# Kernel optimization log

Measured on AMD Instinct MI355X. Metric: run time of the kernel, lower is better.

## Reference

```python
import jax, jax.numpy as jnp
import numpy as np

Z = 16384      # batch of points
N_IN = 127     # dim(Rs_in)
N = N_IN + 1   # +1 ones channel since linear=True
K = 128        # dim(Rs_out)
DIM_TS = 2080  # dim(Rs_ts), ~ n(n+1)/2 surviving tensor-square paths
T_DENSITY = 0.05  # CG-like tensor T is sparse


def setup_inputs() -> dict:
    key = jax.random.key(0)
    k1, k2, k3, k4 = jax.random.split(key, 4)
    features = jax.random.normal(k1, (Z, N_IN), dtype=jnp.float32)
    W = jax.random.normal(k2, (K, DIM_TS), dtype=jnp.float32)  # KernelLinear weights
    T = jax.random.normal(k3, (DIM_TS, N * N), dtype=jnp.float32)
    mask = jax.random.uniform(k4, (DIM_TS, N * N)) < T_DENSITY  # emulate sparse CG structure
    T = jnp.where(mask, T, 0.0)
    return {"features": features, "W": W, "T": T}


def reference(features, W, T):
    # features: [Z, n_in]; prepend ones column (linear=True path)
    f = jnp.concatenate(
        [jnp.ones((features.shape[0], 1), dtype=features.dtype), features], axis=1
    )  # [Z, N]
    # kernel = (T.t() @ W.T).T reshaped -> equivalently (W @ T).reshape(K, N, N)
    kernel3 = (W @ T).reshape(K, N, N)
    # out[z,k] = sum_ij kernel3[k,i,j] * f[z,i] * f[z,j]
    return jnp.einsum('kij,zi,zj->zk', kernel3, f, f)
```

## Files before the change

### kernel.cpp

```cpp
#include <hip/hip_runtime.h>


#define ZTOT 16384
#define NIN  127
#define KOUT 128
#define DTS  2080
#define PTOT 16384

typedef _Float16 h8 __attribute__((ext_vector_type(8)));
typedef _Float16 h2 __attribute__((ext_vector_type(2)));
typedef float f32x4 __attribute__((ext_vector_type(4)));
typedef float f32x16 __attribute__((ext_vector_type(16)));

static __device__ __forceinline__ void gl16(const void* g, void* l) {
  __builtin_amdgcn_global_load_lds((const __attribute__((address_space(1))) unsigned int*)g,
                                   (__attribute__((address_space(3))) unsigned int*)l, 16, 0, 0);
}

static __device__ __forceinline__ unsigned int pk16(float a, float b) {
  return __builtin_bit_cast(unsigned int, __builtin_amdgcn_cvt_pkrtz(a, b));
}

__global__ __launch_bounds__(256) void k_wf(const float* __restrict__ W,
                                            _Float16* __restrict__ Wf) {
  const int t = threadIdx.x, lane = t & 63;
  const int unit = blockIdx.x * 4 + (t >> 6);
  if (unit >= 520) return;
  const int s = unit >> 3, kg = unit & 7;
  const int krow = kg * 16 + (lane & 15);
  const int dbase = s * 32 + ((lane >> 4) << 3);
  h8 v;
#pragma unroll
  for (int e = 0; e < 8; ++e) v[e] = (_Float16)W[(size_t)krow * DTS + dbase + e];
  *(h8*)(Wf + ((size_t)unit * 64 + lane) * 8) = v;
}

__global__ __launch_bounds__(256, 2) void k_wt(const float* __restrict__ T,
                                               const _Float16* __restrict__ Wf,
                                               _Float16* __restrict__ K3a,
                                               _Float16* __restrict__ K3b) {
  __shared__ __align__(16) _Float16 Tb0[64 * 32];
  __shared__ __align__(16) _Float16 Tb1[64 * 32];
  const int t = threadIdx.x, lane = t & 63, w = t >> 6;
  const int ptile = (int)blockIdx.x >> 1, chunk = (int)blockIdx.x & 1;
  const int p0 = ptile * 64;
  const int sb = chunk ? 33 : 0, ns = chunk ? 32 : 33;
  _Float16* K3c = chunk ? K3b : K3a;

  const int p4 = t & 15, dp = 2 * (t >> 4);
  const int wbase = 256 * p4 + 16 * ((dp >> 3) ^ (p4 & 3)) + 2 * (dp & 7);
  const int l15 = lane & 15;
  const int su = 16 * ((lane >> 4) ^ (l15 >> 2));

  const float* gT = T + (size_t)(sb * 32 + dp) * PTOT + p0 + 4 * p4;

#define LOADW(Q0, Q1, S)                                      \
  {                                                           \
    const float* gp = gT + (size_t)(S) * (32 * PTOT);         \
    Q0 = *(const float4*)gp;                                  \
    Q1 = *(const float4*)(gp + PTOT);                         \
  }
#define WRITEW(BUF, Q0, Q1)                                   \
  {                                                           \
    char* wb = (char*)(BUF) + wbase;                          \
    *(unsigned int*)(wb + 0)   = pk16(Q0.x, Q1.x);            \
    *(unsigned int*)(wb + 64)  = pk16(Q0.y, Q1.y);            \
    *(unsigned int*)(wb + 128) = pk16(Q0.z, Q1.z);            \
    *(unsigned int*)(wb + 192) = pk16(Q0.w, Q1.w);            \
  }
#define COMPUTEW(BUF, SG)                                                         \
  {                                                                               \
    const _Float16* wfp = Wf + (size_t)(SG) * 4096 + w * 1024 + (size_t)lane * 8; \
    const h8 a0 = *(const h8*)wfp;                                                \
    const h8 a1 = *(const h8*)(wfp + 512);                                        \
    _Pragma("unroll") for (int nf = 0; nf < 4; ++nf) {                            \
      const h8 b = *(const h8*)((const char*)(BUF) + 64 * (nf * 16 + l15) + su);  \
      acc0[nf] = __builtin_amdgcn_mfma_f32_16x16x32_f16(a0, b, acc0[nf], 0, 0, 0); \
      acc1[nf] = __builtin_amdgcn_mfma_f32_16x16x32_f16(a1, b, acc1[nf], 0, 0, 0); \
    }                                                                             \
  }

  f32x4 acc0[4] = {}, acc1[4] = {};
  float4 A0, A1, Br0, Br1;
  LOADW(A0, A1, 0)
  LOADW(Br0, Br1, 1)
  WRITEW(Tb0, A0, A1)
  __syncthreads();
  for (int s = 0; s < ns; s += 2) {
    if (s + 2 < ns) LOADW(A0, A1, s + 2)
    if (s + 1 < ns) WRITEW(Tb1, Br0, Br1)
    COMPUTEW(Tb0, sb + s)
    __syncthreads();
    if (s + 1 < ns) {
      if (s + 3 < ns) LOADW(Br0, Br1, s + 3)
      if (s + 2 < ns) WRITEW(Tb0, A0, A1)
      COMPUTEW(Tb1, sb + s + 1)
      __syncthreads();
    }
  }
  const int rb = (lane >> 4) << 2;
#pragma unroll
  for (int nf = 0; nf < 4; ++nf)
#pragma unroll
    for (int r = 0; r < 4; ++r) {
      K3c[(size_t)(w * 32 + rb + r) * PTOT + p0 + nf * 16 + l15] = (_Float16)acc0[nf][r];
      K3c[(size_t)(w * 32 + 16 + rb + r) * PTOT + p0 + nf * 16 + l15] = (_Float16)acc1[nf][r];
    }
#undef LOADW
#undef WRITEW
#undef COMPUTEW
}

__global__ __launch_bounds__(256) void k_sum(const _Float16* __restrict__ A,
                                             const _Float16* __restrict__ B,
                                             _Float16* __restrict__ O) {
  const size_t i = ((size_t)blockIdx.x * 256 + threadIdx.x) * 8;
  const h8 a = *(const h8*)(A + i);
  const h8 b = *(const h8*)(B + i);
  *(h8*)(O + i) = a + b;
}

__global__ __launch_bounds__(256, 2) void k_qf(const float* __restrict__ features,
                                               const _Float16* __restrict__ K3,
                                               float* __restrict__ out) {
  __shared__ __align__(16) _Float16 B0[16384];
  __shared__ __align__(16) _Float16 B1[16384];
  __shared__ _Float16 fT[32 * 136];
  const int t = threadIdx.x, lane = t & 63, w = t >> 6;
  const int zg = w >> 1, kg = w & 1, hg = lane >> 5, l31 = lane & 31;
  const int zb = blockIdx.x >> 2, ic = blockIdx.x & 3;
  const int z0 = zb * 128, i0 = ic * 32;

  {
    const int row = t >> 1, hf = t & 1;
    const float* fr = features + (size_t)(z0 + row) * NIN;
    const int rs = (row & 7) << 4;
#pragma unroll
    for (int qb = 0; qb < 8; ++qb) {
      h8 v;
#pragma unroll
      for (int e = 0; e < 8; ++e) {
        const int j = hf * 64 + qb * 8 + e;
        v[e] = (j == 0) ? (_Float16)1.0f : (_Float16)fr[j - 1];
      }
      *(h8*)((char*)B0 + row * 256 + (((hf * 8 + qb) * 16) ^ rs)) = v;
    }
  }
  {
    const int z = t >> 1, ih = t & 1;
#pragma unroll
    for (int q = 0; q < 16; ++q) {
      const int il = ih * 16 + q, gi = i0 + il;
      const float fv = (gi == 0) ? 1.0f : features[(size_t)(z0 + z) * NIN + gi - 1];
      fT[il * 136 + z] = (_Float16)fv;
    }
  }
  __syncthreads();

  h8 fj8[2][8];
#pragma unroll
  for (int m = 0; m < 2; ++m) {
    const int rowm = zg * 64 + m * 32 + l31;
    const int rs = (rowm & 7) << 4;
#pragma unroll
    for (int kc = 0; kc < 8; ++kc)
      fj8[m][kc] = *(const h8*)((const char*)B0 + rowm * 256 + (((kc * 2 + hg) * 16) ^ rs));
  }
  __syncthreads();

  const _Float16* Kbase = K3 + (size_t)i0 * 128;
#define STAGE_B(BUF, IPH)                                                      \
  {                                                                            \
    const _Float16* src = Kbase + (IPH) * 128;                                 \
    _Pragma("unroll") for (int r = 0; r < 8; ++r) {                            \
      const int Lb = r * 4096 + w * 1024;                                      \
      const int row = (Lb >> 8) + (lane >> 4);                                 \
      const int us = (lane & 15) ^ (row & 7);                                  \
      gl16(src + (size_t)row * PTOT + us * 8, (char*)(BUF) + Lb);              \
    }                                                                          \
  }

  f32x16 acc[2][2] = {};
  STAGE_B(B0, 0)
  __syncthreads();

  const int rs0 = (l31 & 7) << 4;
  const int brow0 = (kg * 64 + l31) * 256;
  const int brow1 = (kg * 64 + 32 + l31) * 256;

#define PHASE(CURB, NXTB, PH, DO_STAGE)                                        \
  {                                                                            \
    if (DO_STAGE) STAGE_B(NXTB, (PH) + 1)                                      \
    const _Float16 f0 = fT[(PH) * 136 + zg * 64 + l31];                        \
    const _Float16 f1 = fT[(PH) * 136 + zg * 64 + 32 + l31];                   \
    const h2 fi0 = {f0, f0};                                                   \
    const h2 fi1 = {f1, f1};                                                   \
    _Pragma("unroll") for (int kc = 0; kc < 8; ++kc) {                         \
      const int uoff = ((kc * 2 + hg) * 16) ^ rs0;                             \
      const h8 b0 = *(const h8*)((const char*)(CURB) + brow0 + uoff);          \
      const h8 b1 = *(const h8*)((const char*)(CURB) + brow1 + uoff);          \
      h8 a0, a1;                                                               \
      _Pragma("unroll") for (int r = 0; r < 4; ++r) {                          \
        const h2 j0 = {fj8[0][kc][2 * r], fj8[0][kc][2 * r + 1]};              \
        const h2 j1 = {fj8[1][kc][2 * r], fj8[1][kc][2 * r + 1]};              \
        const h2 p0 = fi0 * j0;                                                \
        const h2 p1 = fi1 * j1;                                                \
        a0[2 * r] = p0[0]; a0[2 * r + 1] = p0[1];                              \
        a1[2 * r] = p1[0]; a1[2 * r + 1] = p1[1];                              \
      }                                                                        \
      acc[0][0] = __builtin_amdgcn_mfma_f32_32x32x16_f16(a0, b0, acc[0][0], 0, 0, 0); \
      acc[0][1] = __builtin_amdgcn_mfma_f32_32x32x16_f16(a0, b1, acc[0][1], 0, 0, 0); \
      acc[1][0] = __builtin_amdgcn_mfma_f32_32x32x16_f16(a1, b0, acc[1][0], 0, 0, 0); \
      acc[1][1] = __builtin_amdgcn_mfma_f32_32x32x16_f16(a1, b1, acc[1][1], 0, 0, 0); \
    }                                                                          \
    __syncthreads();                                                           \
  }

  for (int pb = 0; pb < 16; ++pb) {
    PHASE(B0, B1, pb * 2, true)
    PHASE(B1, B0, pb * 2 + 1, (pb < 15))
  }

  const int kq = kg * 64 + l31;
#pragma unroll
  for (int m = 0; m < 2; ++m)
#pragma unroll
    for (int n = 0; n < 2; ++n)
#pragma unroll
      for (int r = 0; r < 16; ++r) {
        const int zr = (r & 3) + ((r >> 2) << 3) + (hg << 2);
        const int z = z0 + zg * 64 + m * 32 + zr;
        atomicAdd(out + (size_t)z * KOUT + kq + n * 32, acc[m][n][r]);
      }
}

extern "C" void kernel_launch(void* const* d_in, const int* in_sizes, int n_in,
                              void* d_out, int out_size, void* d_ws, size_t ws_size,
                              hipStream_t stream) {
  const float* features = (const float*)d_in[0];
  const float* W        = (const float*)d_in[1];
  const float* T        = (const float*)d_in[2];
  float* out = (float*)d_out;

  _Float16* K3h = (_Float16*)d_ws;
  _Float16* Wf  = K3h + (size_t)2 * 1024 * 1024;
  _Float16* K3a = (_Float16*)d_out;
  _Float16* K3b = K3a + (size_t)2 * 1024 * 1024;

  k_wf<<<dim3(130), dim3(256), 0, stream>>>(W, Wf);
  k_wt<<<dim3(512), dim3(256), 0, stream>>>(T, Wf, K3a, K3b);
  k_sum<<<dim3(1024), dim3(256), 0, stream>>>(K3a, K3b, K3h);
  (void)hipMemsetAsync(d_out, 0, (size_t)ZTOT * KOUT * sizeof(float), stream);
  k_qf<<<dim3(512), dim3(256), 0, stream>>>(features, K3h, out);
}
```

Baseline: 289.6 us.

## Shrink tiles and LDS in W@T and quadratic-form kernels to raise occupancy

The W@T kernel now uses 32-column p-tiles, launching 1024 blocks. Each block stages 64 d-rows per step, so every wave issues two sets of MFMAs per barrier, and the leftover 2048..2079 slice is handled in a tail on the second chunk. The quadratic-form kernel moves to 512-thread blocks with half-size LDS buffers. It stages K3 in half-row (64-column) pieces and drops the transposed fT buffer, reading each f_i straight from global memory one step ahead. The aim is more resident waves for latency hiding, at the cost of more barriers and smaller per-wave MFMA tiles.

```diff
diff --git a/kernel.cpp b/kernel.cpp
--- a/kernel.cpp
+++ b/kernel.cpp
@@ -35,72 +35,99 @@
   *(h8*)(Wf + ((size_t)unit * 64 + lane) * 8) = v;
 }
 
-__global__ __launch_bounds__(256, 2) void k_wt(const float* __restrict__ T,
+__global__ __launch_bounds__(256, 4) void k_wt(const float* __restrict__ T,
                                                const _Float16* __restrict__ Wf,
                                                _Float16* __restrict__ K3a,
                                                _Float16* __restrict__ K3b) {
-  __shared__ __align__(16) _Float16 Tb0[64 * 32];
-  __shared__ __align__(16) _Float16 Tb1[64 * 32];
+  __shared__ __align__(16) _Float16 Tb0[32 * 64];
+  __shared__ __align__(16) _Float16 Tb1[32 * 64];
   const int t = threadIdx.x, lane = t & 63, w = t >> 6;
   const int ptile = (int)blockIdx.x >> 1, chunk = (int)blockIdx.x & 1;
-  const int p0 = ptile * 64;
-  const int sb = chunk ? 33 : 0, ns = chunk ? 32 : 33;
+  const int p0 = ptile * 32;
+  const int dbase = chunk ? 1024 : 0;
   _Float16* K3c = chunk ? K3b : K3a;
 
-  const int p4 = t & 15, dp = 2 * (t >> 4);
-  const int wbase = 256 * p4 + 16 * ((dp >> 3) ^ (p4 & 3)) + 2 * (dp & 7);
+  const int g = t & 127, h = t >> 7;
+  const int p4 = g & 7, dp = 2 * (g >> 3);
+  const int dloc = h * 32 + dp;
+  const int u0w = dloc >> 3, bin = 2 * (dp & 7);
   const int l15 = lane & 15;
-  const int su = 16 * ((lane >> 4) ^ (l15 >> 2));
-
-  const float* gT = T + (size_t)(sb * 32 + dp) * PTOT + p0 + 4 * p4;
-
-#define LOADW(Q0, Q1, S)                                      \
-  {                                                           \
-    const float* gp = gT + (size_t)(S) * (32 * PTOT);         \
-    Q0 = *(const float4*)gp;                                  \
-    Q1 = *(const float4*)(gp + PTOT);                         \
-  }
-#define WRITEW(BUF, Q0, Q1)                                   \
-  {                                                           \
-    char* wb = (char*)(BUF) + wbase;                          \
-    *(unsigned int*)(wb + 0)   = pk16(Q0.x, Q1.x);            \
-    *(unsigned int*)(wb + 64)  = pk16(Q0.y, Q1.y);            \
-    *(unsigned int*)(wb + 128) = pk16(Q0.z, Q1.z);            \
-    *(unsigned int*)(wb + 192) = pk16(Q0.w, Q1.w);            \
-  }
-#define COMPUTEW(BUF, SG)                                                         \
-  {                                                                               \
-    const _Float16* wfp = Wf + (size_t)(SG) * 4096 + w * 1024 + (size_t)lane * 8; \
-    const h8 a0 = *(const h8*)wfp;                                                \
-    const h8 a1 = *(const h8*)(wfp + 512);                                        \
-    _Pragma("unroll") for (int nf = 0; nf < 4; ++nf) {                            \
-      const h8 b = *(const h8*)((const char*)(BUF) + 64 * (nf * 16 + l15) + su);  \
-      acc0[nf] = __builtin_amdgcn_mfma_f32_16x16x32_f16(a0, b, acc0[nf], 0, 0, 0); \
-      acc1[nf] = __builtin_amdgcn_mfma_f32_16x16x32_f16(a1, b, acc1[nf], 0, 0, 0); \
-    }                                                                             \
-  }
-
-  f32x4 acc0[4] = {}, acc1[4] = {};
-  float4 A0, A1, Br0, Br1;
+
+  const float* gT = T + (size_t)(dbase + dloc) * PTOT + p0 + 4 * p4;
+
+#define LOADW(Q0, Q1, S)                                  \
+  {                                                       \
+    const float* gp = gT + (size_t)(S) * (64 * PTOT);     \
+    Q0 = *(const float4*)gp;                              \
+    Q1 = *(const float4*)(gp + PTOT);                     \
+  }
+#define WRITEW(BUF, Q0, Q1)                                             \
+  {                                                                     \
+    char* wb = (char*)(BUF);                                            \
+    const int pr0 = p4 * 4;                                             \
+    *(unsigned int*)(wb + (pr0 + 0) * 128 + ((u0w ^ ((pr0 + 0) & 7)) << 4) + bin) = pk16(Q0.x, Q1.x); \
+    *(unsigned int*)(wb + (pr0 + 1) * 128 + ((u0w ^ ((pr0 + 1) & 7)) << 4) + bin) = pk16(Q0.y, Q1.y); \
+    *(unsigned int*)(wb + (pr0 + 2) * 128 + ((u0w ^ ((pr0 + 2) & 7)) << 4) + bin) = pk16(Q0.z, Q1.z); \
+    *(unsigned int*)(wb + (pr0 + 3) * 128 + ((u0w ^ ((pr0 + 3) & 7)) << 4) + bin) = pk16(Q0.w, Q1.w); \
+  }
+#define COMPUTEW(BUF, SGBASE)                                                        \
+  {                                                                                  \
+    _Pragma("unroll") for (int sg = 0; sg < 2; ++sg) {                               \
+      const _Float16* wfp = Wf + (size_t)((SGBASE) + sg) * 4096 + w * 1024 + (size_t)lane * 8; \
+      const h8 a0 = *(const h8*)wfp;                                                 \
+      const h8 a1 = *(const h8*)(wfp + 512);                                         \
+      _Pragma("unroll") for (int nf = 0; nf < 2; ++nf) {                             \
+        const int row = nf * 16 + l15;                                               \
+        const int u = (sg * 4 + (lane >> 4)) ^ (l15 & 7);                            \
+        const h8 b = *(const h8*)((const char*)(BUF) + row * 128 + (u << 4));        \
+        acc0[nf] = __builtin_amdgcn_mfma_f32_16x16x32_f16(a0, b, acc0[nf], 0, 0, 0); \
+        acc1[nf] = __builtin_amdgcn_mfma_f32_16x16x32_f16(a1, b, acc1[nf], 0, 0, 0); \
+      }                                                                              \
+    }                                                                                \
+  }
+
+  f32x4 acc0[2] = {}, acc1[2] = {};
+  float4 A0, A1, B0r, B1r, T0r, T1r;
+  const int sgb = dbase >> 5;
   LOADW(A0, A1, 0)
-  LOADW(Br0, Br1, 1)
+  LOADW(B0r, B1r, 1)
   WRITEW(Tb0, A0, A1)
   __syncthreads();
-  for (int s = 0; s < ns; s += 2) {
-    if (s + 2 < ns) LOADW(A0, A1, s + 2)
-    if (s + 1 < ns) WRITEW(Tb1, Br0, Br1)
-    COMPUTEW(Tb0, sb + s)
-    __syncthreads();
-    if (s + 1 < ns) {
-      if (s + 3 < ns) LOADW(Br0, Br1, s + 3)
-      if (s + 2 < ns) WRITEW(Tb0, A0, A1)
-      COMPUTEW(Tb1, sb + s + 1)
-      __syncthreads();
+  for (int s = 0; s < 16; s += 2) {
+    if (s + 2 < 16) LOADW(A0, A1, s + 2)
+    if (s + 2 == 16 && chunk && t < 128) {
+      const float* gp = T + (size_t)(2048 + dp) * PTOT + p0 + 4 * p4;
+      T0r = *(const float4*)gp;
+      T1r = *(const float4*)(gp + PTOT);
+    }
+    WRITEW(Tb1, B0r, B1r)
+    COMPUTEW(Tb0, sgb + s * 2)
+    __syncthreads();
+    if (s + 3 < 16) LOADW(B0r, B1r, s + 3)
+    if (s + 2 < 16) WRITEW(Tb0, A0, A1)
+    COMPUTEW(Tb1, sgb + s * 2 + 2)
+    __syncthreads();
+  }
+  if (chunk) {
+    if (t < 128) WRITEW(Tb0, T0r, T1r)
+    __syncthreads();
+    {
+      const _Float16* wfp = Wf + (size_t)64 * 4096 + w * 1024 + (size_t)lane * 8;
+      const h8 a0 = *(const h8*)wfp;
+      const h8 a1 = *(const h8*)(wfp + 512);
+#pragma unroll
+      for (int nf = 0; nf < 2; ++nf) {
+        const int row = nf * 16 + l15;
+        const int u = (lane >> 4) ^ (l15 & 7);
+        const h8 b = *(const h8*)((const char*)Tb0 + row * 128 + (u << 4));
+        acc0[nf] = __builtin_amdgcn_mfma_f32_16x16x32_f16(a0, b, acc0[nf], 0, 0, 0);
+        acc1[nf] = __builtin_amdgcn_mfma_f32_16x16x32_f16(a1, b, acc1[nf], 0, 0, 0);
+      }
     }
   }
   const int rb = (lane >> 4) << 2;
 #pragma unroll
-  for (int nf = 0; nf < 4; ++nf)
+  for (int nf = 0; nf < 2; ++nf)
 #pragma unroll
     for (int r = 0; r < 4; ++r) {
       K3c[(size_t)(w * 32 + rb + r) * PTOT + p0 + nf * 16 + l15] = (_Float16)acc0[nf][r];
@@ -120,118 +147,131 @@
   *(h8*)(O + i) = a + b;
 }
 
-__global__ __launch_bounds__(256, 2) void k_qf(const float* __restrict__ features,
+__global__ __launch_bounds__(512, 4) void k_qf(const float* __restrict__ features,
                                                const _Float16* __restrict__ K3,
                                                float* __restrict__ out) {
-  __shared__ __align__(16) _Float16 B0[16384];
-  __shared__ __align__(16) _Float16 B1[16384];
-  __shared__ _Float16 fT[32 * 136];
+  __shared__ __align__(16) _Float16 Bh0[8192];
+  __shared__ __align__(16) _Float16 Bh1[8192];
   const int t = threadIdx.x, lane = t & 63, w = t >> 6;
-  const int zg = w >> 1, kg = w & 1, hg = lane >> 5, l31 = lane & 31;
-  const int zb = blockIdx.x >> 2, ic = blockIdx.x & 3;
-  const int z0 = zb * 128, i0 = ic * 32;
+  const int zg = w >> 2, kg = w & 3, hg = lane >> 5, l31 = lane & 31;
+  const int zb = (int)blockIdx.x >> 2, ic = (int)blockIdx.x & 2 ? ((int)blockIdx.x & 3) : ((int)blockIdx.x & 3);
+  const int ic4 = (int)blockIdx.x & 3;
+  const int z0 = zb * 128, i0 = ic4 * 32;
+  (void)ic;
 
   {
-    const int row = t >> 1, hf = t & 1;
+    const int row = t >> 2, sub = t & 3, rs = row & 7;
     const float* fr = features + (size_t)(z0 + row) * NIN;
-    const int rs = (row & 7) << 4;
-#pragma unroll
-    for (int qb = 0; qb < 8; ++qb) {
+#pragma unroll
+    for (int q = 0; q < 2; ++q) {
       h8 v;
 #pragma unroll
       for (int e = 0; e < 8; ++e) {
-        const int j = hf * 64 + qb * 8 + e;
+        const int j = sub * 16 + q * 8 + e;
         v[e] = (j == 0) ? (_Float16)1.0f : (_Float16)fr[j - 1];
       }
-      *(h8*)((char*)B0 + row * 256 + (((hf * 8 + qb) * 16) ^ rs)) = v;
-    }
-  }
+      *(h8*)((char*)Bh0 + row * 128 + (((sub * 2 + q) ^ rs) << 4)) = v;
+    }
+  }
+  __syncthreads();
   {
-    const int z = t >> 1, ih = t & 1;
-#pragma unroll
-    for (int q = 0; q < 16; ++q) {
-      const int il = ih * 16 + q, gi = i0 + il;
-      const float fv = (gi == 0) ? 1.0f : features[(size_t)(z0 + z) * NIN + gi - 1];
-      fT[il * 136 + z] = (_Float16)fv;
-    }
-  }
-  __syncthreads();
-
-  h8 fj8[2][8];
+    const int row = t >> 2, sub = t & 3, rs = row & 7;
+    const float* fr = features + (size_t)(z0 + row) * NIN;
+#pragma unroll
+    for (int q = 0; q < 2; ++q) {
+      h8 v;
+#pragma unroll
+      for (int e = 0; e < 8; ++e) v[e] = (_Float16)fr[63 + sub * 16 + q * 8 + e];
+      *(h8*)((char*)Bh1 + row * 128 + (((sub * 2 + q) ^ rs) << 4)) = v;
+    }
+  }
+  h8 fj[2][8];
 #pragma unroll
   for (int m = 0; m < 2; ++m) {
-    const int rowm = zg * 64 + m * 32 + l31;
-    const int rs = (rowm & 7) << 4;
-#pragma unroll
-    for (int kc = 0; kc < 8; ++kc)
-      fj8[m][kc] = *(const h8*)((const char*)B0 + rowm * 256 + (((kc * 2 + hg) * 16) ^ rs));
-  }
-  __syncthreads();
-
-  const _Float16* Kbase = K3 + (size_t)i0 * 128;
-#define STAGE_B(BUF, IPH)                                                      \
-  {                                                                            \
-    const _Float16* src = Kbase + (IPH) * 128;                                 \
-    _Pragma("unroll") for (int r = 0; r < 8; ++r) {                            \
-      const int Lb = r * 4096 + w * 1024;                                      \
-      const int row = (Lb >> 8) + (lane >> 4);                                 \
-      const int us = (lane & 15) ^ (row & 7);                                  \
-      gl16(src + (size_t)row * PTOT + us * 8, (char*)(BUF) + Lb);              \
-    }                                                                          \
-  }
-
-  f32x16 acc[2][2] = {};
-  STAGE_B(B0, 0)
-  __syncthreads();
-
-  const int rs0 = (l31 & 7) << 4;
-  const int brow0 = (kg * 64 + l31) * 256;
-  const int brow1 = (kg * 64 + 32 + l31) * 256;
-
-#define PHASE(CURB, NXTB, PH, DO_STAGE)                                        \
-  {                                                                            \
-    if (DO_STAGE) STAGE_B(NXTB, (PH) + 1)                                      \
-    const _Float16 f0 = fT[(PH) * 136 + zg * 64 + l31];                        \
-    const _Float16 f1 = fT[(PH) * 136 + zg * 64 + 32 + l31];                   \
-    const h2 fi0 = {f0, f0};                                                   \
-    const h2 fi1 = {f1, f1};                                                   \
-    _Pragma("unroll") for (int kc = 0; kc < 8; ++kc) {                         \
-      const int uoff = ((kc * 2 + hg) * 16) ^ rs0;                             \
-      const h8 b0 = *(const h8*)((const char*)(CURB) + brow0 + uoff);          \
-      const h8 b1 = *(const h8*)((const char*)(CURB) + brow1 + uoff);          \
-      h8 a0, a1;                                                               \
-      _Pragma("unroll") for (int r = 0; r < 4; ++r) {                          \
-        const h2 j0 = {fj8[0][kc][2 * r], fj8[0][kc][2 * r + 1]};              \
-        const h2 j1 = {fj8[1][kc][2 * r], fj8[1][kc][2 * r + 1]};              \
-        const h2 p0 = fi0 * j0;                                                \
-        const h2 p1 = fi1 * j1;                                                \
-        a0[2 * r] = p0[0]; a0[2 * r + 1] = p0[1];                              \
-        a1[2 * r] = p1[0]; a1[2 * r + 1] = p1[1];                              \
-      }                                                                        \
-      acc[0][0] = __builtin_amdgcn_mfma_f32_32x32x16_f16(a0, b0, acc[0][0], 0, 0, 0); \
-      acc[0][1] = __builtin_amdgcn_mfma_f32_32x32x16_f16(a0, b1, acc[0][1], 0, 0, 0); \
-      acc[1][0] = __builtin_amdgcn_mfma_f32_32x32x16_f16(a1, b0, acc[1][0], 0, 0, 0); \
-      acc[1][1] = __builtin_amdgcn_mfma_f32_32x32x16_f16(a1, b1, acc[1][1], 0, 0, 0); \
-    }                                                                          \
-    __syncthreads();                                                           \
-  }
-
-  for (int pb = 0; pb < 16; ++pb) {
-    PHASE(B0, B1, pb * 2, true)
-    PHASE(B1, B0, pb * 2 + 1, (pb < 15))
-  }
-
-  const int kq = kg * 64 + l31;
-#pragma unroll
-  for (int m = 0; m < 2; ++m)
-#pragma unroll
-    for (int n = 0; n < 2; ++n)
-#pragma unroll
-      for (int r = 0; r < 16; ++r) {
-        const int zr = (r & 3) + ((r >> 2) << 3) + (hg << 2);
-        const int z = z0 + zg * 64 + m * 32 + zr;
-        atomicAdd(out + (size_t)z * KOUT + kq + n * 32, acc[m][n][r]);
-      }
+    const int rowm = zg * 64 + m * 32 + l31, rs = rowm & 7;
+#pragma unroll
+    for (int c = 0; c < 4; ++c)
+      fj[m][c] = *(const h8*)((const char*)Bh0 + rowm * 128 + ((((c * 2 + hg)) ^ rs) << 4));
+  }
+  __syncthreads();
+#pragma unroll
+  for (int m = 0; m < 2; ++m) {
+    const int rowm = zg * 64 + m * 32 + l31, rs = rowm & 7;
+#pragma unroll
+    for (int c = 0; c < 4; ++c)
+      fj[m][4 + c] = *(const h8*)((const char*)Bh1 + rowm * 128 + ((((c * 2 + hg)) ^ rs) << 4));
+  }
+
+#define STAGE(BUF, HP)                                                        \
+  {                                                                           \
+    const int i_ = (HP) >> 1, jh_ = (HP) & 1;                                 \
+    const _Float16* src = K3 + (size_t)(i0 + i_) * 128 + jh_ * 64;            \
+    _Pragma("unroll") for (int r = 0; r < 2; ++r) {                           \
+      const int rowb = (w * 2 + r) * 8 + (lane >> 3);                         \
+      gl16(src + (size_t)rowb * PTOT + (((lane & 7) ^ (lane >> 3)) << 3),     \
+           (char*)(BUF) + (w * 2 + r) * 1024);                                \
+    }                                                                         \
+  }
+#define COMPUTE(BUF, CBASE)                                                   \
+  {                                                                           \
+    _Pragma("unroll") for (int kc = 0; kc < 4; ++kc) {                        \
+      const int c = (CBASE) + kc;                                             \
+      const h8 fjA = fj[0][c], fjB = fj[1][c];                                \
+      h8 a0, a1;                                                              \
+      _Pragma("unroll") for (int r = 0; r < 4; ++r) {                         \
+        const h2 j0 = {fjA[2 * r], fjA[2 * r + 1]};                           \
+        const h2 j1 = {fjB[2 * r], fjB[2 * r + 1]};                           \
+        const h2 p0 = fi0 * j0;                                               \
+        const h2 p1 = fi1 * j1;                                               \
+        a0[2 * r] = p0[0]; a0[2 * r + 1] = p0[1];                             \
+        a1[2 * r] = p1[0]; a1[2 * r + 1] = p1[1];                             \
+      }                                                                       \
+      const h8 b = *(const h8*)((const char*)(BUF) + brow +                   \
+                                (((kc * 2 + hg) ^ sl7) << 4));                \
+      acc0 = __builtin_amdgcn_mfma_f32_32x32x16_f16(a0, b, acc0, 0, 0, 0);    \
+      acc1 = __builtin_amdgcn_mfma_f32_32x32x16_f16(a1, b, acc1, 0, 0, 0);    \
+    }                                                                         \
+  }
+
+  const int brow = (kg * 32 + l31) * 128;
+  const int sl7 = l31 & 7;
+  const size_t zrow0 = (size_t)(z0 + zg * 64 + l31) * NIN;
+  const size_t zrow1 = (size_t)(z0 + zg * 64 + 32 + l31) * NIN;
+
+  f32x16 acc0 = {}, acc1 = {};
+  float fn0 = (i0 == 0) ? 1.0f : features[zrow0 + i0 - 1];
+  float fn1 = (i0 == 0) ? 1.0f : features[zrow1 + i0 - 1];
+  STAGE(Bh0, 0)
+  __syncthreads();
+
+  h2 fi0, fi1;
+  for (int pb = 0; pb < 32; ++pb) {
+    {
+      const _Float16 c0 = (_Float16)fn0, c1 = (_Float16)fn1;
+      fi0 = (h2){c0, c0};
+      fi1 = (h2){c1, c1};
+    }
+    if (pb < 31) {
+      fn0 = features[zrow0 + i0 + pb];
+      fn1 = features[zrow1 + i0 + pb];
+    }
+    STAGE(Bh1, 2 * pb + 1)
+    COMPUTE(Bh0, 0)
+    __syncthreads();
+    if (pb < 31) STAGE(Bh0, 2 * pb + 2)
+    COMPUTE(Bh1, 4)
+    __syncthreads();
+  }
+
+  const int kq = kg * 32 + l31;
+#pragma unroll
+  for (int r = 0; r < 16; ++r) {
+    const int zr = (r & 3) + ((r >> 2) << 3) + (hg << 2);
+    atomicAdd(out + (size_t)(z0 + zg * 64 + zr) * KOUT + kq, acc0[r]);
+    atomicAdd(out + (size_t)(z0 + zg * 64 + 32 + zr) * KOUT + kq, acc1[r]);
+  }
+#undef STAGE
+#undef COMPUTE
 }
 
 extern "C" void kernel_launch(void* const* d_in, const int* in_sizes, int n_in,
@@ -248,8 +288,8 @@
   _Float16* K3b = K3a + (size_t)2 * 1024 * 1024;
 
   k_wf<<<dim3(130), dim3(256), 0, stream>>>(W, Wf);
-  k_wt<<<dim3(512), dim3(256), 0, stream>>>(T, Wf, K3a, K3b);
+  k_wt<<<dim3(1024), dim3(256), 0, stream>>>(T, Wf, K3a, K3b);
   k_sum<<<dim3(1024), dim3(256), 0, stream>>>(K3a, K3b, K3h);
   (void)hipMemsetAsync(d_out, 0, (size_t)ZTOT * KOUT * sizeof(float), stream);
-  k_qf<<<dim3(512), dim3(256), 0, stream>>>(features, K3h, out);
-}
+  k_qf<<<dim3(512), dim3(512), 0, stream>>>(features, K3h, out);
+}
```

Result: slower. 320.8 us (+10.8%).

## Deepen K3 staging to 4-stage half-tile ring with vmcnt-gated barriers

Applied to the files above, without the earlier changes.

The quadratic-form kernel now stages K3 in half-tiles (64 columns) through a four-slot LDS ring, keeping three global->LDS loads in flight. Each phase waits on a counted vmcnt instead of a full sync, and raises wave priority around the MFMA block. The A-fragment products are built before the barrier so they overlap the load wait. The W-transform kernel replaces __syncthreads with a barrier that waits only on lgkmcnt. The hand-counted vmcnt values and manual barriers give up compiler safety in exchange for deeper overlap of loads with compute.

```diff
diff --git a/kernel.cpp b/kernel.cpp
--- a/kernel.cpp
+++ b/kernel.cpp
@@ -20,6 +20,13 @@
 static __device__ __forceinline__ unsigned int pk16(float a, float b) {
   return __builtin_bit_cast(unsigned int, __builtin_amdgcn_cvt_pkrtz(a, b));
 }
+
+#define BARW                                                \
+  {                                                         \
+    asm volatile("s_waitcnt lgkmcnt(0)" ::: "memory");      \
+    __builtin_amdgcn_s_barrier();                           \
+    __builtin_amdgcn_sched_barrier(0);                      \
+  }
 
 __global__ __launch_bounds__(256) void k_wf(const float* __restrict__ W,
                                             _Float16* __restrict__ Wf) {
@@ -85,17 +92,17 @@
   LOADW(A0, A1, 0)
   LOADW(Br0, Br1, 1)
   WRITEW(Tb0, A0, A1)
-  __syncthreads();
+  BARW
   for (int s = 0; s < ns; s += 2) {
     if (s + 2 < ns) LOADW(A0, A1, s + 2)
     if (s + 1 < ns) WRITEW(Tb1, Br0, Br1)
     COMPUTEW(Tb0, sb + s)
-    __syncthreads();
+    BARW
     if (s + 1 < ns) {
       if (s + 3 < ns) LOADW(Br0, Br1, s + 3)
       if (s + 2 < ns) WRITEW(Tb0, A0, A1)
       COMPUTEW(Tb1, sb + s + 1)
-      __syncthreads();
+      BARW
     }
   }
   const int rb = (lane >> 4) << 2;
@@ -123,12 +130,11 @@
 __global__ __launch_bounds__(256, 2) void k_qf(const float* __restrict__ features,
                                                const _Float16* __restrict__ K3,
                                                float* __restrict__ out) {
-  __shared__ __align__(16) _Float16 B0[16384];
-  __shared__ __align__(16) _Float16 B1[16384];
+  __shared__ __align__(16) _Float16 Bq[32768];
   __shared__ _Float16 fT[32 * 136];
   const int t = threadIdx.x, lane = t & 63, w = t >> 6;
   const int zg = w >> 1, kg = w & 1, hg = lane >> 5, l31 = lane & 31;
-  const int zb = blockIdx.x >> 2, ic = blockIdx.x & 3;
+  const int zb = (int)blockIdx.x >> 2, ic = (int)blockIdx.x & 3;
   const int z0 = zb * 128, i0 = ic * 32;
 
   {
@@ -143,7 +149,7 @@
         const int j = hf * 64 + qb * 8 + e;
         v[e] = (j == 0) ? (_Float16)1.0f : (_Float16)fr[j - 1];
       }
-      *(h8*)((char*)B0 + row * 256 + (((hf * 8 + qb) * 16) ^ rs)) = v;
+      *(h8*)((char*)Bq + row * 256 + (((hf * 8 + qb) * 16) ^ rs)) = v;
     }
   }
   {
@@ -163,63 +169,77 @@
     const int rowm = zg * 64 + m * 32 + l31;
     const int rs = (rowm & 7) << 4;
 #pragma unroll
-    for (int kc = 0; kc < 8; ++kc)
-      fj8[m][kc] = *(const h8*)((const char*)B0 + rowm * 256 + (((kc * 2 + hg) * 16) ^ rs));
+    for (int c = 0; c < 8; ++c)
+      fj8[m][c] = *(const h8*)((const char*)Bq + rowm * 256 + (((c * 2 + hg) * 16) ^ rs));
   }
   __syncthreads();
 
-  const _Float16* Kbase = K3 + (size_t)i0 * 128;
-#define STAGE_B(BUF, IPH)                                                      \
-  {                                                                            \
-    const _Float16* src = Kbase + (IPH) * 128;                                 \
-    _Pragma("unroll") for (int r = 0; r < 8; ++r) {                            \
-      const int Lb = r * 4096 + w * 1024;                                      \
-      const int row = (Lb >> 8) + (lane >> 4);                                 \
-      const int us = (lane & 15) ^ (row & 7);                                  \
-      gl16(src + (size_t)row * PTOT + us * 8, (char*)(BUF) + Lb);              \
-    }                                                                          \
-  }
-
+  const int sl7 = l31 & 7;
+  const int brow0 = (kg * 64 + l31) * 128;
+  const int brow1 = (kg * 64 + 32 + l31) * 128;
   f32x16 acc[2][2] = {};
-  STAGE_B(B0, 0)
-  __syncthreads();
-
-  const int rs0 = (l31 & 7) << 4;
-  const int brow0 = (kg * 64 + l31) * 256;
-  const int brow1 = (kg * 64 + 32 + l31) * 256;
-
-#define PHASE(CURB, NXTB, PH, DO_STAGE)                                        \
-  {                                                                            \
-    if (DO_STAGE) STAGE_B(NXTB, (PH) + 1)                                      \
-    const _Float16 f0 = fT[(PH) * 136 + zg * 64 + l31];                        \
-    const _Float16 f1 = fT[(PH) * 136 + zg * 64 + 32 + l31];                   \
-    const h2 fi0 = {f0, f0};                                                   \
-    const h2 fi1 = {f1, f1};                                                   \
-    _Pragma("unroll") for (int kc = 0; kc < 8; ++kc) {                         \
-      const int uoff = ((kc * 2 + hg) * 16) ^ rs0;                             \
-      const h8 b0 = *(const h8*)((const char*)(CURB) + brow0 + uoff);          \
-      const h8 b1 = *(const h8*)((const char*)(CURB) + brow1 + uoff);          \
-      h8 a0, a1;                                                               \
-      _Pragma("unroll") for (int r = 0; r < 4; ++r) {                          \
-        const h2 j0 = {fj8[0][kc][2 * r], fj8[0][kc][2 * r + 1]};              \
-        const h2 j1 = {fj8[1][kc][2 * r], fj8[1][kc][2 * r + 1]};              \
-        const h2 p0 = fi0 * j0;                                                \
-        const h2 p1 = fi1 * j1;                                                \
-        a0[2 * r] = p0[0]; a0[2 * r + 1] = p0[1];                              \
-        a1[2 * r] = p1[0]; a1[2 * r + 1] = p1[1];                              \
-      }                                                                        \
-      acc[0][0] = __builtin_amdgcn_mfma_f32_32x32x16_f16(a0, b0, acc[0][0], 0, 0, 0); \
-      acc[0][1] = __builtin_amdgcn_mfma_f32_32x32x16_f16(a0, b1, acc[0][1], 0, 0, 0); \
-      acc[1][0] = __builtin_amdgcn_mfma_f32_32x32x16_f16(a1, b0, acc[1][0], 0, 0, 0); \
-      acc[1][1] = __builtin_amdgcn_mfma_f32_32x32x16_f16(a1, b1, acc[1][1], 0, 0, 0); \
-    }                                                                          \
-    __syncthreads();                                                           \
-  }
-
-  for (int pb = 0; pb < 16; ++pb) {
-    PHASE(B0, B1, pb * 2, true)
-    PHASE(B1, B0, pb * 2 + 1, (pb < 15))
-  }
+
+#define STAGEQ(BI, P)                                                            \
+  {                                                                              \
+    const _Float16* src = K3 + (size_t)(i0 + ((P) >> 1)) * 128 + ((P) & 1) * 64; \
+    _Pragma("unroll") for (int r = 0; r < 4; ++r) {                              \
+      const int rowb = w * 32 + r * 8 + (lane >> 3);                             \
+      gl16(src + (size_t)rowb * PTOT + (((lane & 7) ^ (lane >> 3)) << 3),        \
+           (char*)Bq + (BI) * 16384 + w * 4096 + r * 1024);                      \
+    }                                                                            \
+  }
+
+#define PHASEQ(BI, CB, IPH, DOST, SP, VM)                                        \
+  {                                                                              \
+    if (DOST) STAGEQ((SP) & 3, SP)                                               \
+    const _Float16 f0s = fT[(IPH) * 136 + zg * 64 + l31];                        \
+    const _Float16 f1s = fT[(IPH) * 136 + zg * 64 + 32 + l31];                   \
+    const h2 fi0 = {f0s, f0s};                                                   \
+    const h2 fi1 = {f1s, f1s};                                                   \
+    h8 a0[4], a1[4];                                                             \
+    _Pragma("unroll") for (int kl = 0; kl < 4; ++kl) {                           \
+      const h8 fjA = fj8[0][(CB) + kl], fjB = fj8[1][(CB) + kl];                 \
+      _Pragma("unroll") for (int r = 0; r < 4; ++r) {                            \
+        const h2 j0 = {fjA[2 * r], fjA[2 * r + 1]};                              \
+        const h2 j1 = {fjB[2 * r], fjB[2 * r + 1]};                              \
+        const h2 q0 = fi0 * j0;                                                  \
+        const h2 q1 = fi1 * j1;                                                  \
+        a0[kl][2 * r] = q0[0]; a0[kl][2 * r + 1] = q0[1];                        \
+        a1[kl][2 * r] = q1[0]; a1[kl][2 * r + 1] = q1[1];                        \
+      }                                                                          \
+    }                                                                            \
+    asm volatile("s_waitcnt vmcnt(" #VM ")" ::: "memory");                       \
+    __builtin_amdgcn_s_barrier();                                                \
+    __builtin_amdgcn_sched_barrier(0);                                           \
+    __builtin_amdgcn_s_setprio(1);                                               \
+    const char* bp = (const char*)Bq + (BI) * 16384;                             \
+    _Pragma("unroll") for (int kl = 0; kl < 4; ++kl) {                           \
+      const int ur = ((kl * 2 + hg) ^ sl7) << 4;                                 \
+      const h8 b0 = *(const h8*)(bp + brow0 + ur);                               \
+      const h8 b1 = *(const h8*)(bp + brow1 + ur);                               \
+      acc[0][0] = __builtin_amdgcn_mfma_f32_32x32x16_f16(a0[kl], b0, acc[0][0], 0, 0, 0); \
+      acc[0][1] = __builtin_amdgcn_mfma_f32_32x32x16_f16(a0[kl], b1, acc[0][1], 0, 0, 0); \
+      acc[1][0] = __builtin_amdgcn_mfma_f32_32x32x16_f16(a1[kl], b0, acc[1][0], 0, 0, 0); \
+      acc[1][1] = __builtin_amdgcn_mfma_f32_32x32x16_f16(a1[kl], b1, acc[1][1], 0, 0, 0); \
+    }                                                                            \
+    __builtin_amdgcn_s_setprio(0);                                               \
+    __builtin_amdgcn_sched_barrier(0);                                           \
+    __builtin_amdgcn_s_barrier();                                                \
+  }
+
+  STAGEQ(0, 0)
+  STAGEQ(1, 1)
+  STAGEQ(2, 2)
+  for (int pb = 0; pb < 30; ++pb) {
+    PHASEQ((2 * pb) & 3, 0, pb, 1, 2 * pb + 3, 12)
+    PHASEQ((2 * pb + 1) & 3, 4, pb, 1, 2 * pb + 4, 12)
+  }
+  PHASEQ(0, 0, 30, 1, 63, 12)
+  PHASEQ(1, 4, 30, 0, 0, 8)
+  PHASEQ(2, 0, 31, 0, 0, 4)
+  PHASEQ(3, 4, 31, 0, 0, 0)
+#undef STAGEQ
+#undef PHASEQ
 
   const int kq = kg * 64 + l31;
 #pragma unroll
```

Measured after the change: 299.1 us. 1.03x slower.
